# Kernel tuning notes

Measured on AMD Instinct MI355X. Metric: run time of the kernel, lower is better.

## Reference

```python
import jax, jax.numpy as jnp
import numpy as np

# Problem dims
B, C, H, W = 4, 64, 32, 32          # input
O, G, CS = 128, 4, 64               # out channels, clusters per oc, cluster size
KH = KW = 3
PAD, STRIDE = 1, 1
SEG = C * KH * KW                   # 576, valid range for col_idx
E = O * G * CS                      # 32768 gathered columns


def setup_inputs() -> dict:
    key = jax.random.key(0)
    k1, k2, k3 = jax.random.split(key, 3)
    x = jax.random.normal(k1, (B, C, H, W), dtype=jnp.float32)
    means = jax.random.normal(k2, (O, G), dtype=jnp.float32) * 0.1
    bias = jax.random.normal(k3, (O,), dtype=jnp.float32) * 0.01
    rng = np.random.default_rng(0)
    # Each (oc, g) cluster owns CS random patch-row indices in [0, SEG)
    col_idx = jnp.asarray(rng.integers(0, SEG, size=(E,)), dtype=jnp.int32)
    # dest = oc * G + g, CS entries per cluster (matches torch buffer construction)
    dest = jnp.asarray(np.repeat(np.arange(O * G, dtype=np.int32), CS))
    return {"x": x, "means": means, "bias": bias, "col_idx": col_idx, "dest": dest}


def _unfold(x):
    # torch.nn.functional.unfold equivalent: [B, C*KH*KW, Ho*Wo], channel-major (c slowest)
    Ho = (H + 2 * PAD - KH) // STRIDE + 1
    Wo = (W + 2 * PAD - KW) // STRIDE + 1
    xp = jnp.pad(x, ((0, 0), (0, 0), (PAD, PAD), (PAD, PAD)))
    cols = [xp[:, :, kh:kh + STRIDE * Ho:STRIDE, kw:kw + STRIDE * Wo:STRIDE]
            for kh in range(KH) for kw in range(KW)]
    p = jnp.stack(cols, axis=2)                      # [B, C, KH*KW, Ho, Wo]
    return p.reshape(B, C * KH * KW, Ho * Wo), Ho, Wo


def reference(x, means, bias, col_idx, dest):
    patches, Ho, Wo = _unfold(x)                     # [B, SEG, HW]
    src = patches[:, col_idx, :]                     # gather -> [B, E, HW]
    HWn = src.shape[-1]
    # scatter-add over edges into (oc, g) segments
    sums = jax.ops.segment_sum(
        src.transpose(1, 0, 2).reshape(E, B * HWn), dest, num_segments=O * G)
    sums = sums.reshape(O, G, B, HWn)                # [O, G, B, HW]
    y = jnp.einsum('ogbh,og->boh', sums, means)      # weighted sum over clusters
    return y.reshape(B, O, Ho, Wo) + bias[None, :, None, None]
```

## Files before the change

### kernel.cpp

```cpp
#include <hip/hip_runtime.h>

typedef __attribute__((ext_vector_type(8))) short bf16x8;
typedef __attribute__((ext_vector_type(4))) float f32x4;

constexpr int kB   = 4;
constexpr int kC   = 64;
constexpr int kH   = 32;
constexpr int kW   = 32;
constexpr int kO   = 128;
constexpr int kG   = 4;
constexpr int kHW  = kH * kW;
constexpr int kSEG = kC * 9;

__device__ __forceinline__ unsigned short f2bf(float f) {
    union { float f; unsigned u; } v; v.f = f;
    const unsigned r = v.u + 0x7FFFu + ((v.u >> 16) & 1u);
    return (unsigned short)(r >> 16);
}

__global__ __launch_bounds__(256) void build_w_kernel(
    const float* __restrict__ means,
    const int*   __restrict__ col_idx,
    unsigned short* __restrict__ Wg)
{
    __shared__ float wacc[kSEG];
    const int o = blockIdx.x, t = threadIdx.x;

    for (int i = t; i < kSEG; i += 256) wacc[i] = 0.f;
    __syncthreads();

    const int s = col_idx[o * 256 + t];
    atomicAdd(&wacc[s], means[o * kG + (t >> 6)]);
    __syncthreads();

    for (int i = t; i < kSEG; i += 256) {
        const int tap = i >> 6;
        const int ch  = i & 63;
        Wg[o * kSEG + i] = f2bf(wacc[ch * 9 + tap]);
    }
}

__global__ __launch_bounds__(256) void conv_mfma_kernel(
    const float* __restrict__ x,
    const unsigned short* __restrict__ Wg,
    const float* __restrict__ bias,
    float* __restrict__ out)
{
    __shared__ unsigned short xs[4 * 34 * 72];

    const int bi  = blockIdx.x;
    const int ot  = bi >> 6;
    const int pxb = bi & 63;
    const int b   = pxb >> 4;
    const int rp  = pxb & 15;
    const int t   = threadIdx.x;
    const int w   = t >> 6;
    const int ln  = t & 63;
    const int ln15 = ln & 15;
    const int g    = ln >> 4;
    const int wr   = w >> 1;
    const int c0   = (w & 1) * 16;

    const unsigned short* wp = Wg + (ot * 16 + ln15) * kSEG + g * 8;
    bf16x8 bfr[18];
    #pragma unroll
    for (int s = 0; s < 18; ++s)
        bfr[s] = *reinterpret_cast<const bf16x8*>(wp + s * 32);

    {
        const int cp    = t >> 3;
        const int r4    = (t >> 1) & 3;
        const int chalf = t & 1;
        const int ch0   = cp * 2;
        const int hr    = rp * 2 - 1 + r4;
        const bool rowok = (hr >= 0) && (hr < kH);
        const float* x0 = x + (((size_t)b * kC + ch0) * kH + (rowok ? hr : 0)) * kW;
        const float* x1 = x0 + kHW;
        const int hcb = chalf * 16;

        float4 f0[4], f1[4];
        #pragma unroll
        for (int q = 0; q < 4; ++q) {
            f0[q] = rowok ? *reinterpret_cast<const float4*>(x0 + hcb + q * 4)
                          : make_float4(0.f, 0.f, 0.f, 0.f);
            f1[q] = rowok ? *reinterpret_cast<const float4*>(x1 + hcb + q * 4)
                          : make_float4(0.f, 0.f, 0.f, 0.f);
        }

        if (chalf == 0) {
            #pragma unroll
            for (int j = 0; j < 17; ++j) {
                float v0 = 0.f, v1 = 0.f;
                if (j > 0) {
                    const int h = j - 1;
                    v0 = reinterpret_cast<const float*>(&f0[h >> 2])[h & 3];
                    v1 = reinterpret_cast<const float*>(&f1[h >> 2])[h & 3];
                }
                const unsigned pkv =
                    (unsigned)f2bf(v0) | ((unsigned)f2bf(v1) << 16);
                *reinterpret_cast<unsigned*>(
                    &xs[(r4 * 34 + j) * 72 + ch0]) = pkv;
            }
        } else {
            #pragma unroll
            for (int j = 0; j < 17; ++j) {
                float v0 = 0.f, v1 = 0.f;
                if (j < 16) {
                    v0 = reinterpret_cast<const float*>(&f0[j >> 2])[j & 3];
                    v1 = reinterpret_cast<const float*>(&f1[j >> 2])[j & 3];
                }
                const unsigned pkv =
                    (unsigned)f2bf(v0) | ((unsigned)f2bf(v1) << 16);
                *reinterpret_cast<unsigned*>(
                    &xs[(r4 * 34 + 17 + j) * 72 + ch0]) = pkv;
            }
        }
    }
    __syncthreads();

    f32x4 acc = {0.f, 0.f, 0.f, 0.f};
    #pragma unroll
    for (int s = 0; s < 18; ++s) {
        const int tap  = s >> 1;
        const int half = s & 1;
        const int kh   = tap / 3;
        const int kw   = tap % 3;
        const int r4   = wr + kh;
        const int c34  = c0 + ln15 + kw;
        const bf16x8 a = *reinterpret_cast<const bf16x8*>(
            &xs[(r4 * 34 + c34) * 72 + half * 32 + g * 8]);
        acc = __builtin_amdgcn_mfma_f32_16x16x32_bf16(a, bfr[s], acc, 0, 0, 0);
    }

    const int o     = ot * 16 + ln15;
    const float bo  = bias[o];
    const int pxrow = rp * 2 + wr;
    const float4 res = make_float4(acc[0] + bo, acc[1] + bo,
                                   acc[2] + bo, acc[3] + bo);
    *reinterpret_cast<float4*>(
        &out[((size_t)(b * kO + o)) * kHW + pxrow * kW + c0 + g * 4]) = res;
}

__global__ __launch_bounds__(256) void conv_direct_kernel(
    const float* __restrict__ x,
    const float* __restrict__ means,
    const float* __restrict__ bias,
    const int*   __restrict__ col_idx,
    float*       __restrict__ out)
{
    __shared__ float tile[34 * 34];
    __shared__ float wloc[kC * 9];

    const int o = blockIdx.x & (kO - 1);
    const int b = blockIdx.x >> 7;
    const int t = threadIdx.x;

    for (int i = t; i < kC * 9; i += 256) wloc[i] = 0.f;
    __syncthreads();
    {
        const int s = col_idx[o * 256 + t];
        atomicAdd(&wloc[s], means[o * kG + (t >> 6)]);
    }

    const int c  = t & 31;
    const int r0 = (t >> 5) * 4;
    const float* xb = x + (size_t)b * kC * kHW;
    float acc[4] = {0.f, 0.f, 0.f, 0.f};

    for (int ch = 0; ch < kC; ++ch) {
        __syncthreads();
        for (int i = t; i < 34 * 34; i += 256) {
            const int rr = i / 34, cc = i - rr * 34;
            const int hr = rr - 1, hc = cc - 1;
            float v = 0.f;
            if (hr >= 0 && hr < kH && hc >= 0 && hc < kW)
                v = xb[ch * kHW + hr * kW + hc];
            tile[i] = v;
        }
        __syncthreads();
        float wv[9];
        #pragma unroll
        for (int k = 0; k < 9; ++k) wv[k] = wloc[ch * 9 + k];
        float xv[6][3];
        #pragma unroll
        for (int i = 0; i < 6; ++i)
            #pragma unroll
            for (int j = 0; j < 3; ++j)
                xv[i][j] = tile[(r0 + i) * 34 + c + j];
        #pragma unroll
        for (int i = 0; i < 4; ++i)
            #pragma unroll
            for (int kh = 0; kh < 3; ++kh)
                #pragma unroll
                for (int kw = 0; kw < 3; ++kw)
                    acc[i] += wv[kh * 3 + kw] * xv[i + kh][kw];
    }
    const float bo = bias[o];
    #pragma unroll
    for (int i = 0; i < 4; ++i)
        out[((size_t)b * kO + o) * kHW + (r0 + i) * kW + c] = acc[i] + bo;
}

extern "C" void kernel_launch(void* const* d_in, const int* in_sizes, int n_in,
                              void* d_out, int out_size, void* d_ws, size_t ws_size,
                              hipStream_t stream)
{
    const float* x       = (const float*)d_in[0];
    const float* means   = (const float*)d_in[1];
    const float* bias    = (const float*)d_in[2];
    const int*   col_idx = (const int*)d_in[3];
    float*       out     = (float*)d_out;

    constexpr size_t kWBytes = (size_t)kO * kSEG * sizeof(unsigned short);

    if (ws_size >= kWBytes) {
        unsigned short* Wg = (unsigned short*)d_ws;
        build_w_kernel<<<kO, 256, 0, stream>>>(means, col_idx, Wg);
        conv_mfma_kernel<<<512, 256, 0, stream>>>(x, Wg, bias, out);
    } else {
        conv_direct_kernel<<<kB * kO, 256, 0, stream>>>(
            x, means, bias, col_idx, out);
    }
}
```

Before: 17.78 us.

## Fuse weight-building into MFMA conv kernel, eliminating separate launch

Each conv block now rebuilds the 16 output channels' dense bf16 weights in shared memory itself, using LDS atomics over col_idx and means, instead of reading a weight matrix written to workspace by a separate kernel. This removes one kernel launch and the global write/read round trip between the two kernels. The cost is redundant weight building, since 64 blocks share each output tile, plus about 37KB of extra LDS that may reduce occupancy. The direct fallback path is deleted.

```diff
diff --git a/kernel.cpp b/kernel.cpp
--- a/kernel.cpp
+++ b/kernel.cpp
@@ -11,6 +11,7 @@
 constexpr int kG   = 4;
 constexpr int kHW  = kH * kW;
 constexpr int kSEG = kC * 9;
+constexpr int kWS  = 580;
 
 __device__ __forceinline__ unsigned short f2bf(float f) {
     union { float f; unsigned u; } v; v.f = f;
@@ -18,35 +19,16 @@
     return (unsigned short)(r >> 16);
 }
 
-__global__ __launch_bounds__(256) void build_w_kernel(
+__global__ __launch_bounds__(256) void conv_fused_kernel(
+    const float* __restrict__ x,
     const float* __restrict__ means,
+    const float* __restrict__ bias,
     const int*   __restrict__ col_idx,
-    unsigned short* __restrict__ Wg)
-{
-    __shared__ float wacc[kSEG];
-    const int o = blockIdx.x, t = threadIdx.x;
-
-    for (int i = t; i < kSEG; i += 256) wacc[i] = 0.f;
-    __syncthreads();
-
-    const int s = col_idx[o * 256 + t];
-    atomicAdd(&wacc[s], means[o * kG + (t >> 6)]);
-    __syncthreads();
-
-    for (int i = t; i < kSEG; i += 256) {
-        const int tap = i >> 6;
-        const int ch  = i & 63;
-        Wg[o * kSEG + i] = f2bf(wacc[ch * 9 + tap]);
-    }
-}
-
-__global__ __launch_bounds__(256) void conv_mfma_kernel(
-    const float* __restrict__ x,
-    const unsigned short* __restrict__ Wg,
-    const float* __restrict__ bias,
     float* __restrict__ out)
 {
+    __shared__ float wacc[16 * kWS];
     __shared__ unsigned short xs[4 * 34 * 72];
+    __shared__ float mloc[64];
 
     const int bi  = blockIdx.x;
     const int ot  = bi >> 6;
@@ -61,32 +43,56 @@
     const int wr   = w >> 1;
     const int c0   = (w & 1) * 16;
 
-    const unsigned short* wp = Wg + (ot * 16 + ln15) * kSEG + g * 8;
-    bf16x8 bfr[18];
+    const int4* ci4 = reinterpret_cast<const int4*>(col_idx + ot * 16 * 256);
+    int4 civ[4];
     #pragma unroll
-    for (int s = 0; s < 18; ++s)
-        bfr[s] = *reinterpret_cast<const bf16x8*>(wp + s * 32);
+    for (int q = 0; q < 4; ++q) civ[q] = ci4[q * 256 + t];
+    float mv = 0.f;
+    if (t < 64) mv = means[ot * 64 + t];
+
+    const int cp    = t >> 3;
+    const int r4s   = (t >> 1) & 3;
+    const int chalf = t & 1;
+    const int ch0   = cp * 2;
+    const int hr    = rp * 2 - 1 + r4s;
+    const bool rowok = (hr >= 0) && (hr < kH);
+    const float* x0 = x + (((size_t)b * kC + ch0) * kH + (rowok ? hr : 0)) * kW;
+    const float* x1 = x0 + kHW;
+    const int hcb = chalf * 16;
+
+    float4 f0[4], f1[4];
+    #pragma unroll
+    for (int q = 0; q < 4; ++q) {
+        f0[q] = rowok ? *reinterpret_cast<const float4*>(x0 + hcb + q * 4)
+                      : make_float4(0.f, 0.f, 0.f, 0.f);
+        f1[q] = rowok ? *reinterpret_cast<const float4*>(x1 + hcb + q * 4)
+                      : make_float4(0.f, 0.f, 0.f, 0.f);
+    }
+
+    #pragma unroll
+    for (int q = 0; q < 37; ++q) {
+        const int i = q * 256 + t;
+        if (i < 16 * kWS) wacc[i] = 0.f;
+    }
+    if (t < 64) mloc[t] = mv;
+    __syncthreads();
+
+    #pragma unroll
+    for (int q = 0; q < 4; ++q) {
+        const int e0 = (q * 256 + t) * 4;
+        const int* sv = reinterpret_cast<const int*>(&civ[q]);
+        #pragma unroll
+        for (int j = 0; j < 4; ++j) {
+            const int og = (e0 + j) >> 6;
+            const int s  = sv[j];
+            const int ch = s / 9;
+            const int tap = s - ch * 9;
+            atomicAdd(&wacc[(og >> 2) * kWS + tap * 64 + ch], mloc[og]);
+        }
+    }
+    __syncthreads();
 
     {
-        const int cp    = t >> 3;
-        const int r4    = (t >> 1) & 3;
-        const int chalf = t & 1;
-        const int ch0   = cp * 2;
-        const int hr    = rp * 2 - 1 + r4;
-        const bool rowok = (hr >= 0) && (hr < kH);
-        const float* x0 = x + (((size_t)b * kC + ch0) * kH + (rowok ? hr : 0)) * kW;
-        const float* x1 = x0 + kHW;
-        const int hcb = chalf * 16;
-
-        float4 f0[4], f1[4];
-        #pragma unroll
-        for (int q = 0; q < 4; ++q) {
-            f0[q] = rowok ? *reinterpret_cast<const float4*>(x0 + hcb + q * 4)
-                          : make_float4(0.f, 0.f, 0.f, 0.f);
-            f1[q] = rowok ? *reinterpret_cast<const float4*>(x1 + hcb + q * 4)
-                          : make_float4(0.f, 0.f, 0.f, 0.f);
-        }
-
         if (chalf == 0) {
             #pragma unroll
             for (int j = 0; j < 17; ++j) {
@@ -99,7 +105,7 @@
                 const unsigned pkv =
                     (unsigned)f2bf(v0) | ((unsigned)f2bf(v1) << 16);
                 *reinterpret_cast<unsigned*>(
-                    &xs[(r4 * 34 + j) * 72 + ch0]) = pkv;
+                    &xs[(r4s * 34 + j) * 72 + ch0]) = pkv;
             }
         } else {
             #pragma unroll
@@ -112,9 +118,25 @@
                 const unsigned pkv =
                     (unsigned)f2bf(v0) | ((unsigned)f2bf(v1) << 16);
                 *reinterpret_cast<unsigned*>(
-                    &xs[(r4 * 34 + 17 + j) * 72 + ch0]) = pkv;
+                    &xs[(r4s * 34 + 17 + j) * 72 + ch0]) = pkv;
             }
         }
+    }
+
+    bf16x8 bfr[18];
+    #pragma unroll
+    for (int s = 0; s < 18; ++s) {
+        const int tap  = s >> 1;
+        const int half = s & 1;
+        const float* wp = &wacc[ln15 * kWS + tap * 64 + half * 32 + g * 8];
+        const float4 wa = *reinterpret_cast<const float4*>(wp);
+        const float4 wb = *reinterpret_cast<const float4*>(wp + 4);
+        bf16x8 r;
+        r[0] = (short)f2bf(wa.x); r[1] = (short)f2bf(wa.y);
+        r[2] = (short)f2bf(wa.z); r[3] = (short)f2bf(wa.w);
+        r[4] = (short)f2bf(wb.x); r[5] = (short)f2bf(wb.y);
+        r[6] = (short)f2bf(wb.z); r[7] = (short)f2bf(wb.w);
+        bfr[s] = r;
     }
     __syncthreads();
 
@@ -141,66 +163,6 @@
         &out[((size_t)(b * kO + o)) * kHW + pxrow * kW + c0 + g * 4]) = res;
 }
 
-__global__ __launch_bounds__(256) void conv_direct_kernel(
-    const float* __restrict__ x,
-    const float* __restrict__ means,
-    const float* __restrict__ bias,
-    const int*   __restrict__ col_idx,
-    float*       __restrict__ out)
-{
-    __shared__ float tile[34 * 34];
-    __shared__ float wloc[kC * 9];
-
-    const int o = blockIdx.x & (kO - 1);
-    const int b = blockIdx.x >> 7;
-    const int t = threadIdx.x;
-
-    for (int i = t; i < kC * 9; i += 256) wloc[i] = 0.f;
-    __syncthreads();
-    {
-        const int s = col_idx[o * 256 + t];
-        atomicAdd(&wloc[s], means[o * kG + (t >> 6)]);
-    }
-
-    const int c  = t & 31;
-    const int r0 = (t >> 5) * 4;
-    const float* xb = x + (size_t)b * kC * kHW;
-    float acc[4] = {0.f, 0.f, 0.f, 0.f};
-
-    for (int ch = 0; ch < kC; ++ch) {
-        __syncthreads();
-        for (int i = t; i < 34 * 34; i += 256) {
-            const int rr = i / 34, cc = i - rr * 34;
-            const int hr = rr - 1, hc = cc - 1;
-            float v = 0.f;
-            if (hr >= 0 && hr < kH && hc >= 0 && hc < kW)
-                v = xb[ch * kHW + hr * kW + hc];
-            tile[i] = v;
-        }
-        __syncthreads();
-        float wv[9];
-        #pragma unroll
-        for (int k = 0; k < 9; ++k) wv[k] = wloc[ch * 9 + k];
-        float xv[6][3];
-        #pragma unroll
-        for (int i = 0; i < 6; ++i)
-            #pragma unroll
-            for (int j = 0; j < 3; ++j)
-                xv[i][j] = tile[(r0 + i) * 34 + c + j];
-        #pragma unroll
-        for (int i = 0; i < 4; ++i)
-            #pragma unroll
-            for (int kh = 0; kh < 3; ++kh)
-                #pragma unroll
-                for (int kw = 0; kw < 3; ++kw)
-                    acc[i] += wv[kh * 3 + kw] * xv[i + kh][kw];
-    }
-    const float bo = bias[o];
-    #pragma unroll
-    for (int i = 0; i < 4; ++i)
-        out[((size_t)b * kO + o) * kHW + (r0 + i) * kW + c] = acc[i] + bo;
-}
-
 extern "C" void kernel_launch(void* const* d_in, const int* in_sizes, int n_in,
                               void* d_out, int out_size, void* d_ws, size_t ws_size,
                               hipStream_t stream)
@@ -211,14 +173,5 @@
     const int*   col_idx = (const int*)d_in[3];
     float*       out     = (float*)d_out;
 
-    constexpr size_t kWBytes = (size_t)kO * kSEG * sizeof(unsigned short);
-
-    if (ws_size >= kWBytes) {
-        unsigned short* Wg = (unsigned short*)d_ws;
-        build_w_kernel<<<kO, 256, 0, stream>>>(means, col_idx, Wg);
-        conv_mfma_kernel<<<512, 256, 0, stream>>>(x, Wg, bias, out);
-    } else {
-        conv_direct_kernel<<<kB * kO, 256, 0, stream>>>(
-            x, means, bias, col_idx, out);
-    }
+    conv_fused_kernel<<<512, 256, 0, stream>>>(x, means, bias, col_idx, out);
 }
```

Result: slower. 20.48 us (+15.2%).

## Enlarge MFMA conv tiles to 4 output rows and stage weights in LDS

Applied to the files above, without the earlier changes.

The MFMA conv kernel now runs 256 blocks of 512 threads, each computing 4 output rows instead of 2, so the input halo fraction per tile drops (6 staged rows for 4 outputs instead of 4 for 2). The block's 16x576 bf16 weight slice is copied cooperatively into padded shared memory with coalesced 16-byte loads, and each wave then reads its B fragments from LDS instead of doing strided per-lane global loads. Block order is reordered so output-channel tiles are adjacent, which may improve input reuse in L2. The cost is fewer, larger blocks with more LDS, which lowers the number of resident blocks and the parallelism available on a large GPU.

```diff
diff --git a/kernel.cpp b/kernel.cpp
--- a/kernel.cpp
+++ b/kernel.cpp
@@ -11,6 +11,7 @@
 constexpr int kG   = 4;
 constexpr int kHW  = kH * kW;
 constexpr int kSEG = kC * 9;
+constexpr int kWL  = 584;
 
 __device__ __forceinline__ unsigned short f2bf(float f) {
     union { float f; unsigned u; } v; v.f = f;
@@ -40,39 +41,47 @@
     }
 }
 
-__global__ __launch_bounds__(256) void conv_mfma_kernel(
+__global__ __launch_bounds__(512) void conv_mfma_kernel(
     const float* __restrict__ x,
     const unsigned short* __restrict__ Wg,
     const float* __restrict__ bias,
     float* __restrict__ out)
 {
-    __shared__ unsigned short xs[4 * 34 * 72];
+    __shared__ unsigned short xs[6 * 34 * 72];
+    __shared__ unsigned short wl[16 * kWL];
 
     const int bi  = blockIdx.x;
-    const int ot  = bi >> 6;
-    const int pxb = bi & 63;
-    const int b   = pxb >> 4;
-    const int rp  = pxb & 15;
+    const int ot  = bi & 7;
+    const int pxb = bi >> 3;
+    const int b   = pxb >> 3;
+    const int rq  = pxb & 7;
     const int t   = threadIdx.x;
     const int w   = t >> 6;
     const int ln  = t & 63;
     const int ln15 = ln & 15;
     const int g    = ln >> 4;
-    const int wr   = w >> 1;
+    const int prl  = w >> 1;
     const int c0   = (w & 1) * 16;
 
-    const unsigned short* wp = Wg + (ot * 16 + ln15) * kSEG + g * 8;
-    bf16x8 bfr[18];
-    #pragma unroll
-    for (int s = 0; s < 18; ++s)
-        bfr[s] = *reinterpret_cast<const bf16x8*>(wp + s * 32);
-
     {
-        const int cp    = t >> 3;
-        const int r4    = (t >> 1) & 3;
+        const uint4* wg4 = reinterpret_cast<const uint4*>(Wg + ot * 16 * kSEG);
+        #pragma unroll
+        for (int p = 0; p < 3; ++p) {
+            const int c = t + p * 512;
+            if (c < 1152) {
+                const int row = c / 72;
+                const int col = c - row * 72;
+                *reinterpret_cast<uint4*>(&wl[row * kWL + col * 8]) = wg4[c];
+            }
+        }
+    }
+
+    if (t < 384) {
+        const int row6  = t >> 6;
+        const int cp    = (t & 63) >> 1;
         const int chalf = t & 1;
         const int ch0   = cp * 2;
-        const int hr    = rp * 2 - 1 + r4;
+        const int hr    = rq * 4 - 1 + row6;
         const bool rowok = (hr >= 0) && (hr < kH);
         const float* x0 = x + (((size_t)b * kC + ch0) * kH + (rowok ? hr : 0)) * kW;
         const float* x1 = x0 + kHW;
@@ -99,7 +108,7 @@
                 const unsigned pkv =
                     (unsigned)f2bf(v0) | ((unsigned)f2bf(v1) << 16);
                 *reinterpret_cast<unsigned*>(
-                    &xs[(r4 * 34 + j) * 72 + ch0]) = pkv;
+                    &xs[(row6 * 34 + j) * 72 + ch0]) = pkv;
             }
         } else {
             #pragma unroll
@@ -112,11 +121,17 @@
                 const unsigned pkv =
                     (unsigned)f2bf(v0) | ((unsigned)f2bf(v1) << 16);
                 *reinterpret_cast<unsigned*>(
-                    &xs[(r4 * 34 + 17 + j) * 72 + ch0]) = pkv;
+                    &xs[(row6 * 34 + 17 + j) * 72 + ch0]) = pkv;
             }
         }
     }
     __syncthreads();
+
+    bf16x8 bfr[18];
+    #pragma unroll
+    for (int s = 0; s < 18; ++s)
+        bfr[s] = *reinterpret_cast<const bf16x8*>(
+            &wl[ln15 * kWL + s * 32 + g * 8]);
 
     f32x4 acc = {0.f, 0.f, 0.f, 0.f};
     #pragma unroll
@@ -125,16 +140,16 @@
         const int half = s & 1;
         const int kh   = tap / 3;
         const int kw   = tap % 3;
-        const int r4   = wr + kh;
+        const int r6   = prl + kh;
         const int c34  = c0 + ln15 + kw;
         const bf16x8 a = *reinterpret_cast<const bf16x8*>(
-            &xs[(r4 * 34 + c34) * 72 + half * 32 + g * 8]);
+            &xs[(r6 * 34 + c34) * 72 + half * 32 + g * 8]);
         acc = __builtin_amdgcn_mfma_f32_16x16x32_bf16(a, bfr[s], acc, 0, 0, 0);
     }
 
     const int o     = ot * 16 + ln15;
     const float bo  = bias[o];
-    const int pxrow = rp * 2 + wr;
+    const int pxrow = rq * 4 + prl;
     const float4 res = make_float4(acc[0] + bo, acc[1] + bo,
                                    acc[2] + bo, acc[3] + bo);
     *reinterpret_cast<float4*>(
@@ -216,7 +231,7 @@
     if (ws_size >= kWBytes) {
         unsigned short* Wg = (unsigned short*)d_ws;
         build_w_kernel<<<kO, 256, 0, stream>>>(means, col_idx, Wg);
-        conv_mfma_kernel<<<512, 256, 0, stream>>>(x, Wg, bias, out);
+        conv_mfma_kernel<<<256, 512, 0, stream>>>(x, Wg, bias, out);
     } else {
         conv_direct_kernel<<<kB * kO, 256, 0, stream>>>(
             x, means, bias, col_idx, out);
```

After: 14.81 us (median of 2 runs). 16.7% less time.
